# Kernel tuning notes

Measured on AMD Instinct MI355X. Metric: run time of the kernel, lower is better.

## Reference

```python
import jax, jax.numpy as jnp
import numpy as np

DIM = 128; NH = 4; HD = DIM // NH; WS = 7; SS = 3
H1, W1 = 64, 32            # int(256/(224/56)), int(128/(224/56))
PAD_B = (WS - H1 % WS) % WS
PAD_R = (WS - W1 % WS) % WS
H, W = H1 + PAD_B, W1 + PAD_R   # 70, 35
NWIN = (H // WS) * (W // WS)    # 50 windows
N = WS * WS                      # 49 tokens per window
SCALE = HD ** -0.5


def _rel_pos_index():
    c = np.stack(np.meshgrid(np.arange(WS), np.arange(WS), indexing='ij')).reshape(2, -1)
    r = (c[:, :, None] - c[:, None, :]).transpose(1, 2, 0)
    r[:, :, 0] += WS - 1; r[:, :, 1] += WS - 1; r[:, :, 0] *= 2 * WS - 1
    return jnp.asarray(r.sum(-1))  # [N, N] int


def _attn_mask():
    img = np.zeros((H, W), np.float32); cnt = 0
    for h0, h1 in [(0, H - WS), (H - WS, H - SS), (H - SS, H)]:
        for w0, w1 in [(0, W - WS), (W - WS, W - SS), (W - SS, W)]:
            img[h0:h1, w0:w1] = cnt; cnt += 1
    mw = img.reshape(H // WS, WS, W // WS, WS).transpose(0, 2, 1, 3).reshape(-1, N)
    am = mw[:, None, :] - mw[:, :, None]
    return jnp.asarray(np.where(am != 0, -100.0, 0.0).astype(np.float32))  # [NWIN, N, N]


REL_IDX = _rel_pos_index()
ATTN_MASK = _attn_mask()


def _ln(x, g, b):
    m = x.mean(-1, keepdims=True)
    v = jnp.var(x, axis=-1, keepdims=True)
    return (x - m) * jax.lax.rsqrt(v + 1e-5) * g + b


def setup_inputs() -> dict:
    key = jax.random.key(0)
    ks = jax.random.split(key, 8)
    s = 0.02
    return {
        'x': jax.random.normal(ks[0], (64, H1 * W1, DIM), jnp.float32),
        'norm1_g': jnp.ones((DIM,), jnp.float32),
        'norm1_b': jnp.zeros((DIM,), jnp.float32),
        'qkv_w': jax.random.normal(ks[1], (DIM, 3 * DIM), jnp.float32) * s,
        'qkv_b': jnp.zeros((3 * DIM,), jnp.float32),
        'rpb': jax.random.normal(ks[2], ((2 * WS - 1) ** 2, NH), jnp.float32) * s,
        'proj_w': jax.random.normal(ks[3], (DIM, DIM), jnp.float32) * s,
        'proj_b': jnp.zeros((DIM,), jnp.float32),
        'norm2_g': jnp.ones((DIM,), jnp.float32),
        'norm2_b': jnp.zeros((DIM,), jnp.float32),
        'fc1_w': jax.random.normal(ks[4], (DIM, 4 * DIM), jnp.float32) * s,
        'fc1_b': jnp.zeros((4 * DIM,), jnp.float32),
        'fc2_w': jax.random.normal(ks[5], (4 * DIM, DIM), jnp.float32) * s,
        'fc2_b': jnp.zeros((DIM,), jnp.float32),
    }


def reference(x, norm1_g, norm1_b, qkv_w, qkv_b, rpb, proj_w, proj_b,
              norm2_g, norm2_b, fc1_w, fc1_b, fc2_w, fc2_b):
    B, L, C = x.shape
    x = x.reshape(B, H1, W1, C)
    x = jnp.pad(x, ((0, 0), (0, PAD_B), (0, PAD_R), (0, 0)))  # [B,H,W,C]
    shortcut = x.reshape(B, H * W, C)
    xn = _ln(shortcut, norm1_g, norm1_b).reshape(B, H, W, C)
    # cyclic shift
    xs = jnp.roll(xn, (-SS, -SS), axis=(1, 2))
    # window partition -> [B*NWIN, N, C]
    xw = xs.reshape(B, H // WS, WS, W // WS, WS, C).transpose(0, 1, 3, 2, 4, 5).reshape(B * NWIN, N, C)
    # windowed multi-head attention
    qkv = (xw @ qkv_w + qkv_b).reshape(B * NWIN, N, 3, NH, HD).transpose(2, 0, 3, 1, 4)
    q, k, v = qkv[0] * SCALE, qkv[1], qkv[2]            # [B*NWIN, NH, N, HD]
    attn = jnp.einsum('whnd,whmd->whnm', q, k)
    bias = rpb[REL_IDX].transpose(2, 0, 1)              # [NH, N, N]
    attn = attn + bias[None]
    attn = attn.reshape(B, NWIN, NH, N, N) + ATTN_MASK[None, :, None]
    attn = jax.nn.softmax(attn, axis=-1).reshape(B * NWIN, NH, N, N)
    out = jnp.einsum('whnm,whmd->whnd', attn, v).transpose(0, 2, 1, 3).reshape(B * NWIN, N, C)
    out = out @ proj_w + proj_b
    # window reverse + reverse shift
    out = out.reshape(B, H // WS, W // WS, WS, WS, C).transpose(0, 1, 3, 2, 4, 5).reshape(B, H, W, C)
    out = jnp.roll(out, (SS, SS), axis=(1, 2)).reshape(B, H * W, C)
    x = shortcut + out
    # MLP (exact GELU, matching torch default)
    h = _ln(x, norm2_g, norm2_b)
    h = jax.nn.gelu(h @ fc1_w + fc1_b, approximate=False) @ fc2_w + fc2_b
    x = x + h
    # remove padding
    return x.reshape(B, H, W, C)[:, :H1, :W1, :].reshape(B, H1 * W1, C)
```

## Files before the change

kernel.cpp:

```cpp
#include <hip/hip_runtime.h>
#include <hip/hip_bf16.h>

#define B_ 64
#define H1_ 64
#define W1_ 32
#define Hp 70
#define Wp 35
#define C_ 128
#define NH_ 4
#define HD_ 32
#define WS_ 7
#define SS_ 3
#define NWC_ 5
#define NWIN_ 50
#define NTOK_ 49
#define SCALE_ 0.17677669529663687f

typedef __hip_bfloat16 bf16;
typedef __attribute__((ext_vector_type(8))) short sh8;
typedef __attribute__((ext_vector_type(4))) float f32x4;

__device__ __forceinline__ float bs2f(short s) {
    unsigned int u = ((unsigned int)(unsigned short)s) << 16;
    float f; __builtin_memcpy(&f, &u, 4); return f;
}
__device__ __forceinline__ short f2bs(float f) {
    bf16 h = __float2bfloat16(f);
    return *reinterpret_cast<short*>(&h);
}

__global__ void prep_k(const float* __restrict__ qkvw, const float* __restrict__ projw,
                       const float* __restrict__ f1w, const float* __restrict__ f2w,
                       const float* __restrict__ rpb,
                       short* __restrict__ ws) {
    int tid = blockIdx.x * 256 + threadIdx.x;
    if (tid < 49152) {
        int n = tid >> 7, k = tid & 127;
        ws[tid] = f2bs(qkvw[k*384 + n]);
    } else if (tid < 65536) {
        int t = tid - 49152; int n = t >> 7, k = t & 127;
        ws[tid] = f2bs(projw[k*128 + n]);
    } else if (tid < 131072) {
        int t = tid - 65536; int n = t >> 7, k = t & 127;
        ws[tid] = f2bs(f1w[k*512 + n]);
    } else if (tid < 196608) {
        int t = tid - 131072; int n = t >> 9, k = t & 511;
        ws[tid] = f2bs(f2w[k*128 + n]);
    } else if (tid < 212992) {
        int t = tid - 196608;
        int h = t >> 12, i = (t >> 6) & 63, j = t & 63;
        float val = -30000.f;
        if (i < NTOK_ && j < NTOK_) {
            int ri = i / WS_, ci = i % WS_, rj = j / WS_, cj = j % WS_;
            val = rpb[((ri - rj + 6)*13 + (ci - cj + 6))*4 + h];
        }
        ws[tid] = f2bs(val);
    }
}

__global__ __launch_bounds__(512, 4) void win_attn(
    const float* __restrict__ x,
    const float* __restrict__ n1g, const float* __restrict__ n1b,
    const float* __restrict__ qkvb, const short* __restrict__ bt,
    const float* __restrict__ projb,
    const short* __restrict__ wq, const short* __restrict__ wp,
    float* __restrict__ out)
{
    __shared__ char smem[71680];
    short* q_s = (short*)smem;
    short* k_s = (short*)(smem + 17408);
    short* cat = (short*)(smem + 17408);
    short* vt  = (short*)(smem + 34816);
    short* xsp = (short*)(smem + 53248);
    short* p_s = (short*)(smem + 53248);

    const int tid = threadIdx.x;
    const int lane = tid & 63, wv = tid >> 6;
    const int l15 = lane & 15, l4 = lane >> 4;
    const int mt = wv & 3, hg = wv >> 2;
    const int bw = blockIdx.x;
    const int b = bw / NWIN_, win = bw % NWIN_;
    const int wr = win / NWC_, wc = win % NWC_;

    #pragma unroll
    for (int it = 0; it < 4; ++it) {
        int n = it*16 + wv*2 + (lane >> 5);
        int r = n / WS_, cc = n % WS_;
        int h = (wr*WS_ + r + SS_) % Hp;
        int w = (wc*WS_ + cc + SS_) % Wp;
        int c0 = (lane & 31) * 4;
        float4 v = make_float4(0.f, 0.f, 0.f, 0.f);
        if (n < NTOK_ && h < H1_ && w < W1_)
            v = *(const float4*)(x + ((size_t)(b*H1_*W1_ + h*W1_ + w))*C_ + c0);
        float s  = v.x + v.y + v.z + v.w;
        float sq = v.x*v.x + v.y*v.y + v.z*v.z + v.w*v.w;
        #pragma unroll
        for (int off = 1; off < 32; off <<= 1) {
            s  += __shfl_xor(s, off);
            sq += __shfl_xor(sq, off);
        }
        float mean = s * (1.f/128.f);
        float var  = sq * (1.f/128.f) - mean*mean;
        float rstd = rsqrtf(var + 1e-5f);
        short4 o;
        o.x = f2bs((v.x - mean)*rstd*n1g[c0+0] + n1b[c0+0]);
        o.y = f2bs((v.y - mean)*rstd*n1g[c0+1] + n1b[c0+1]);
        o.z = f2bs((v.z - mean)*rstd*n1g[c0+2] + n1b[c0+2]);
        o.w = f2bs((v.w - mean)*rstd*n1g[c0+3] + n1b[c0+3]);
        *(short4*)(xsp + n*136 + c0) = o;
    }
    __syncthreads();

    {
        sh8 bq[4], bqn[4];
        {
            int n0 = (wv*3)*16 + l15;
            #pragma unroll
            for (int kk = 0; kk < 4; ++kk)
                bq[kk] = *(const sh8*)(wq + n0*C_ + kk*32 + l4*8);
        }
        for (int t = 0; t < 3; ++t) {
            int n0 = (wv*3 + t)*16 + l15;
            if (t < 2) {
                int n1 = n0 + 16;
                #pragma unroll
                for (int kk = 0; kk < 4; ++kk)
                    bqn[kk] = *(const sh8*)(wq + n1*C_ + kk*32 + l4*8);
            }
            int mat = n0 >> 7, c = n0 & 127;
            float bias = qkvb[n0];
            float scl = (mat == 0) ? SCALE_ : 1.f;
            #pragma unroll
            for (int mt4 = 0; mt4 < 4; ++mt4) {
                f32x4 acc = {0.f,0.f,0.f,0.f};
                #pragma unroll
                for (int kk = 0; kk < 4; ++kk) {
                    sh8 av = *(const sh8*)(xsp + (mt4*16 + l15)*136 + kk*32 + l4*8);
                    acc = __builtin_amdgcn_mfma_f32_16x16x32_bf16(av, bq[kk], acc, 0,0,0);
                }
                #pragma unroll
                for (int r = 0; r < 4; ++r) {
                    int m0 = mt4*16 + l4*4 + r;
                    float vc = (acc[r] + bias) * scl;
                    if (mat == 0)      q_s[m0*136 + c] = f2bs(vc);
                    else if (mat == 1) k_s[m0*136 + c] = f2bs(vc);
                    else               vt[c*72 + m0]   = f2bs(vc);
                }
            }
            #pragma unroll
            for (int kk = 0; kk < 4; ++kk) bq[kk] = bqn[kk];
        }
    }
    __syncthreads();

    int zi_r[4];
    #pragma unroll
    for (int r = 0; r < 4; ++r) {
        int i = mt*16 + l4*4 + r;
        int ri = i / WS_, ci = i % WS_;
        int hi = wr*WS_ + ri, wi = wc*WS_ + ci;
        zi_r[r] = (hi < 63 ? 0 : (hi < 67 ? 1 : 2))*3 + (wi < 28 ? 0 : (wi < 32 ? 1 : 2));
    }
    int zj_n[4];
    #pragma unroll
    for (int nt = 0; nt < 4; ++nt) {
        int j = nt*16 + l15;
        int rj = j / WS_, cj = j % WS_;
        int hj = wr*WS_ + rj, wj = wc*WS_ + cj;
        zj_n[nt] = (hj < 63 ? 0 : (hj < 67 ? 1 : 2))*3 + (wj < 28 ? 0 : (wj < 32 ? 1 : 2));
    }

    short* myp = p_s + wv*16*72;
    f32x4 o_acc[2][2] = {};
    #pragma unroll
    for (int hl = 0; hl < 2; ++hl) {
        const int h = hg*2 + hl;
        sh8 aq = *(const sh8*)(q_s + (mt*16 + l15)*136 + h*HD_ + l4*8);
        f32x4 s[4];
        __builtin_amdgcn_s_setprio(1);
        #pragma unroll
        for (int nt = 0; nt < 4; ++nt) {
            sh8 bk = *(const sh8*)(k_s + (nt*16 + l15)*136 + h*HD_ + l4*8);
            f32x4 z = {0.f,0.f,0.f,0.f};
            s[nt] = __builtin_amdgcn_mfma_f32_16x16x32_bf16(aq, bk, z, 0,0,0);
        }
        __builtin_amdgcn_s_setprio(0);
        #pragma unroll
        for (int r = 0; r < 4; ++r) {
            const short* btrow = bt + ((size_t)(h*64 + mt*16 + l4*4 + r))*64 + l15;
            #pragma unroll
            for (int nt = 0; nt < 4; ++nt) {
                float sv = s[nt][r] + bs2f(btrow[nt*16]);
                if (zi_r[r] != zj_n[nt]) sv -= 100.f;
                s[nt][r] = sv;
            }
        }
        #pragma unroll
        for (int r = 0; r < 4; ++r) {
            float m0 = fmaxf(fmaxf(s[0][r], s[1][r]), fmaxf(s[2][r], s[3][r]));
            #pragma unroll
            for (int off = 1; off < 16; off <<= 1) m0 = fmaxf(m0, __shfl_xor(m0, off));
            float ls = 0.f;
            #pragma unroll
            for (int nt = 0; nt < 4; ++nt) {
                float e = __expf(s[nt][r] - m0);
                s[nt][r] = e; ls += e;
            }
            #pragma unroll
            for (int off = 1; off < 16; off <<= 1) ls += __shfl_xor(ls, off);
            float inv = 1.f / ls;
            #pragma unroll
            for (int nt = 0; nt < 4; ++nt)
                myp[(l4*4 + r)*72 + nt*16 + l15] = f2bs(s[nt][r] * inv);
        }
        sh8 ap0 = *(const sh8*)(myp + l15*72 + l4*8);
        sh8 ap1 = *(const sh8*)(myp + l15*72 + 32 + l4*8);
        __builtin_amdgcn_s_setprio(1);
        #pragma unroll
        for (int nt2 = 0; nt2 < 2; ++nt2) {
            sh8 bv0 = *(const sh8*)(vt + (h*HD_ + nt2*16 + l15)*72 + l4*8);
            sh8 bv1 = *(const sh8*)(vt + (h*HD_ + nt2*16 + l15)*72 + 32 + l4*8);
            o_acc[hl][nt2] = __builtin_amdgcn_mfma_f32_16x16x32_bf16(ap0, bv0, o_acc[hl][nt2], 0,0,0);
            o_acc[hl][nt2] = __builtin_amdgcn_mfma_f32_16x16x32_bf16(ap1, bv1, o_acc[hl][nt2], 0,0,0);
        }
        __builtin_amdgcn_s_setprio(0);
    }

    __syncthreads();

    #pragma unroll
    for (int hl = 0; hl < 2; ++hl)
        #pragma unroll
        for (int nt2 = 0; nt2 < 2; ++nt2)
            #pragma unroll
            for (int r = 0; r < 4; ++r)
                cat[(mt*16 + l4*4 + r)*136 + (hg*2+hl)*HD_ + nt2*16 + l15] = f2bs(o_acc[hl][nt2][r]);

    bool pred[4]; size_t tokb[4];
    #pragma unroll
    for (int r = 0; r < 4; ++r) {
        int m = mt*16 + l4*4 + r;
        int rr = m / WS_, cc = m % WS_;
        int hh = (wr*WS_ + rr + SS_) % Hp;
        int ww = (wc*WS_ + cc + SS_) % Wp;
        pred[r] = (m < NTOK_) && (hh < H1_) && (ww < W1_);
        tokb[r] = ((size_t)(b*H1_*W1_ + hh*W1_ + ww))*C_;
    }

    sh8 pa[4];
    #pragma unroll
    for (int kk = 0; kk < 4; ++kk)
        pa[kk] = *(const sh8*)(cat + (mt*16 + l15)*136 + kk*32 + l4*8);

    sh8 bpw[4], bpwn[4];
    #pragma unroll
    for (int kk = 0; kk < 4; ++kk)
        bpw[kk] = *(const sh8*)(wp + (hg*64 + l15)*C_ + kk*32 + l4*8);
    for (int nt = 0; nt < 4; ++nt) {
        int ch = hg*64 + nt*16 + l15;
        if (nt < 3) {
            #pragma unroll
            for (int kk = 0; kk < 4; ++kk)
                bpwn[kk] = *(const sh8*)(wp + (ch+16)*C_ + kk*32 + l4*8);
        }
        f32x4 acc = {0.f,0.f,0.f,0.f};
        #pragma unroll
        for (int kk = 0; kk < 4; ++kk)
            acc = __builtin_amdgcn_mfma_f32_16x16x32_bf16(pa[kk], bpw[kk], acc, 0,0,0);
        float pbv = projb[ch];
        #pragma unroll
        for (int r = 0; r < 4; ++r)
            if (pred[r])
                out[tokb[r] + ch] = x[tokb[r] + ch] + acc[r] + pbv;
        #pragma unroll
        for (int kk = 0; kk < 4; ++kk) bpw[kk] = bpwn[kk];
    }
}

__global__ __launch_bounds__(512) void mlp_k(
    float* __restrict__ xio,
    const float* __restrict__ n2g, const float* __restrict__ n2b,
    const float* __restrict__ f1b, const float* __restrict__ f2b,
    const short* __restrict__ w1, const short* __restrict__ w2)
{
    __shared__ char smem[51200];
    float* xin = (float*)smem;
    short* hv  = (short*)smem;
    float* outs= (float*)smem;
    short* h2  = (short*)(smem + 33792);

    const int tid = threadIdx.x;
    const int lane = tid & 63, wv = tid >> 6;
    const int l15 = lane & 15, l4 = lane >> 4;
    const int mh = wv & 1, ng = wv >> 1;
    const size_t base = (size_t)blockIdx.x * 64 * C_;

    for (int i = tid; i < 2048; i += 512) {
        float4 v = ((const float4*)(xio + base))[i];
        int row = i >> 5, col = (i & 31) * 4;
        *(float4*)(xin + row*132 + col) = v;
    }
    __syncthreads();

    {
        int tok = tid >> 3, sub = tid & 7;
        float vbuf[16];
        float s = 0.f, sq = 0.f;
        #pragma unroll
        for (int c = 0; c < 16; ++c) {
            float v = xin[tok*132 + sub*16 + c];
            vbuf[c] = v; s += v; sq += v*v;
        }
        #pragma unroll
        for (int off = 1; off < 8; off <<= 1) {
            s  += __shfl_xor(s, off);
            sq += __shfl_xor(sq, off);
        }
        float mean = s * (1.f/128.f);
        float var  = sq * (1.f/128.f) - mean*mean;
        float rstd = rsqrtf(var + 1e-5f);
        #pragma unroll
        for (int c = 0; c < 16; ++c) {
            int ch = sub*16 + c;
            h2[tok*136 + ch] = f2bs((vbuf[c] - mean)*rstd*n2g[ch] + n2b[ch]);
        }
    }
    float res[2][2][4];
    #pragma unroll
    for (int mt2 = 0; mt2 < 2; ++mt2)
        #pragma unroll
        for (int nt = 0; nt < 2; ++nt)
            #pragma unroll
            for (int r = 0; r < 4; ++r) {
                int m  = (mh*2 + mt2)*16 + l4*4 + r;
                int ch = ng*32 + nt*16 + l15;
                res[mt2][nt][r] = xin[m*132 + ch];
            }
    __syncthreads();

    f32x4 facc[2][2] = {};
    #pragma unroll 1
    for (int chunk = 0; chunk < 2; ++chunk) {
        const int c0 = chunk*256;
        {
            sh8 b1[4], b1n[4];
            #pragma unroll
            for (int kk = 0; kk < 4; ++kk)
                b1[kk] = *(const sh8*)(w1 + (size_t)(c0 + ng*64 + l15)*C_ + kk*32 + l4*8);
            for (int t = 0; t < 4; ++t) {
                int n = c0 + ng*64 + t*16 + l15;
                if (t < 3) {
                    #pragma unroll
                    for (int kk = 0; kk < 4; ++kk)
                        b1n[kk] = *(const sh8*)(w1 + (size_t)(n + 16)*C_ + kk*32 + l4*8);
                }
                float bias = f1b[n];
                #pragma unroll
                for (int mt2 = 0; mt2 < 2; ++mt2) {
                    int mrow = (mh*2 + mt2)*16;
                    f32x4 acc = {0.f,0.f,0.f,0.f};
                    #pragma unroll
                    for (int kk = 0; kk < 4; ++kk) {
                        sh8 av = *(const sh8*)(h2 + (mrow + l15)*136 + kk*32 + l4*8);
                        acc = __builtin_amdgcn_mfma_f32_16x16x32_bf16(av, b1[kk], acc, 0,0,0);
                    }
                    #pragma unroll
                    for (int r = 0; r < 4; ++r) {
                        float xv = acc[r] + bias;
                        float g = xv * 0.5f * (1.f + erff(xv * 0.70710678118654752f));
                        hv[(mrow + l4*4 + r)*264 + ng*64 + t*16 + l15] = f2bs(g);
                    }
                }
                #pragma unroll
                for (int kk = 0; kk < 4; ++kk) b1[kk] = b1n[kk];
            }
        }
        __syncthreads();
        {
            sh8 b2[2], b2n[2];
            #pragma unroll
            for (int nt = 0; nt < 2; ++nt)
                b2[nt] = *(const sh8*)(w2 + (size_t)(ng*32 + nt*16 + l15)*512 + c0 + l4*8);
            for (int ks = 0; ks < 8; ++ks) {
                if (ks < 7) {
                    #pragma unroll
                    for (int nt = 0; nt < 2; ++nt)
                        b2n[nt] = *(const sh8*)(w2 + (size_t)(ng*32 + nt*16 + l15)*512 + c0 + (ks+1)*32 + l4*8);
                }
                #pragma unroll
                for (int mt2 = 0; mt2 < 2; ++mt2) {
                    sh8 av = *(const sh8*)(hv + ((mh*2 + mt2)*16 + l15)*264 + ks*32 + l4*8);
                    facc[mt2][0] = __builtin_amdgcn_mfma_f32_16x16x32_bf16(av, b2[0], facc[mt2][0], 0,0,0);
                    facc[mt2][1] = __builtin_amdgcn_mfma_f32_16x16x32_bf16(av, b2[1], facc[mt2][1], 0,0,0);
                }
                b2[0] = b2n[0]; b2[1] = b2n[1];
            }
        }
        __syncthreads();
    }

    #pragma unroll
    for (int mt2 = 0; mt2 < 2; ++mt2)
        #pragma unroll
        for (int nt = 0; nt < 2; ++nt) {
            int oc = ng*32 + nt*16 + l15;
            float bias = f2b[oc];
            #pragma unroll
            for (int r = 0; r < 4; ++r) {
                int m = (mh*2 + mt2)*16 + l4*4 + r;
                outs[m*132 + oc] = res[mt2][nt][r] + facc[mt2][nt][r] + bias;
            }
        }
    __syncthreads();
    for (int i = tid; i < 2048; i += 512) {
        int row = i >> 5, col = (i & 31) * 4;
        ((float4*)(xio + base))[i] = *(const float4*)(outs + row*132 + col);
    }
}

extern "C" void kernel_launch(void* const* d_in, const int* in_sizes, int n_in,
                              void* d_out, int out_size, void* d_ws, size_t ws_size,
                              hipStream_t stream) {
    const float* x    = (const float*)d_in[0];
    const float* n1g  = (const float*)d_in[1];
    const float* n1b  = (const float*)d_in[2];
    const float* qkvw = (const float*)d_in[3];
    const float* qkvb = (const float*)d_in[4];
    const float* rpb  = (const float*)d_in[5];
    const float* pw   = (const float*)d_in[6];
    const float* pb   = (const float*)d_in[7];
    const float* n2g  = (const float*)d_in[8];
    const float* n2b  = (const float*)d_in[9];
    const float* f1w  = (const float*)d_in[10];
    const float* f1b  = (const float*)d_in[11];
    const float* f2w  = (const float*)d_in[12];
    const float* f2b  = (const float*)d_in[13];

    short* ws = (short*)d_ws;
    const short* wq = ws;
    const short* wp = ws + 49152;
    const short* w1 = ws + 65536;
    const short* w2 = ws + 131072;
    const short* bt = ws + 196608;
    float* xio = (float*)d_out;

    hipLaunchKernelGGL(prep_k, dim3(832), dim3(256), 0, stream, qkvw, pw, f1w, f2w, rpb, ws);
    hipLaunchKernelGGL(win_attn, dim3(B_*NWIN_), dim3(512), 0, stream,
                       x, n1g, n1b, qkvb, bt, pb, wq, wp, xio);
    hipLaunchKernelGGL(mlp_k, dim3(B_*H1_*W1_/64), dim3(512), 0, stream,
                       xio, n2g, n2b, f1b, f2b, w1, w2);
}
```

Before: 307.5 us.

## Compute transposed attention scores and pass probabilities via lane shuffles instead of LDS

Computes S^T with K as the MFMA A operand, so each lane holds a query column. Softmax then reduces over registers plus two cross-row shuffles, and the bf16 probabilities are repacked into the PV A-operand with __shfl rather than a round trip through shared memory. The bias table is stored transposed to match. The residual add of x moves from the attention epilogue into the MLP kernel's load, and an extra barrier is added after the concat write. The aim is to cut LDS traffic and shuffle-reduction steps in exchange for more cross-lane shuffles.

```diff
diff --git a/kernel.cpp b/kernel.cpp
--- a/kernel.cpp
+++ b/kernel.cpp
@@ -27,6 +27,9 @@
 __device__ __forceinline__ short f2bs(float f) {
     bf16 h = __float2bfloat16(f);
     return *reinterpret_cast<short*>(&h);
+}
+__device__ __forceinline__ unsigned pk2(float lo, float hi) {
+    return ((unsigned)(unsigned short)f2bs(hi) << 16) | (unsigned)(unsigned short)f2bs(lo);
 }
 
 __global__ void prep_k(const float* __restrict__ qkvw, const float* __restrict__ projw,
@@ -48,10 +51,10 @@
         ws[tid] = f2bs(f2w[k*128 + n]);
     } else if (tid < 212992) {
         int t = tid - 196608;
-        int h = t >> 12, i = (t >> 6) & 63, j = t & 63;
+        int h = t >> 12, k = (t >> 6) & 63, q = t & 63;
         float val = -30000.f;
-        if (i < NTOK_ && j < NTOK_) {
-            int ri = i / WS_, ci = i % WS_, rj = j / WS_, cj = j % WS_;
+        if (q < NTOK_ && k < NTOK_) {
+            int ri = q / WS_, ci = q % WS_, rj = k / WS_, cj = k % WS_;
             val = rpb[((ri - rj + 6)*13 + (ci - cj + 6))*4 + h];
         }
         ws[tid] = f2bs(val);
@@ -61,18 +64,17 @@
 __global__ __launch_bounds__(512, 4) void win_attn(
     const float* __restrict__ x,
     const float* __restrict__ n1g, const float* __restrict__ n1b,
-    const float* __restrict__ qkvb, const short* __restrict__ bt,
+    const float* __restrict__ qkvb, const short* __restrict__ btT,
     const float* __restrict__ projb,
     const short* __restrict__ wq, const short* __restrict__ wp,
     float* __restrict__ out)
 {
-    __shared__ char smem[71680];
+    __shared__ char smem[70656];
     short* q_s = (short*)smem;
     short* k_s = (short*)(smem + 17408);
     short* cat = (short*)(smem + 17408);
     short* vt  = (short*)(smem + 34816);
     short* xsp = (short*)(smem + 53248);
-    short* p_s = (short*)(smem + 53248);
 
     const int tid = threadIdx.x;
     const int lane = tid & 63, wv = tid >> 6;
@@ -153,77 +155,98 @@
     }
     __syncthreads();
 
-    int zi_r[4];
-    #pragma unroll
-    for (int r = 0; r < 4; ++r) {
-        int i = mt*16 + l4*4 + r;
-        int ri = i / WS_, ci = i % WS_;
-        int hi = wr*WS_ + ri, wi = wc*WS_ + ci;
-        zi_r[r] = (hi < 63 ? 0 : (hi < 67 ? 1 : 2))*3 + (wi < 28 ? 0 : (wi < 32 ? 1 : 2));
-    }
-    int zj_n[4];
-    #pragma unroll
-    for (int nt = 0; nt < 4; ++nt) {
-        int j = nt*16 + l15;
-        int rj = j / WS_, cj = j % WS_;
-        int hj = wr*WS_ + rj, wj = wc*WS_ + cj;
-        zj_n[nt] = (hj < 63 ? 0 : (hj < 67 ? 1 : 2))*3 + (wj < 28 ? 0 : (wj < 32 ? 1 : 2));
-    }
-
-    short* myp = p_s + wv*16*72;
+    int zq;
+    {
+        int qt = mt*16 + l15;
+        int rt = qt / WS_, ct = qt % WS_;
+        int hi = wr*WS_ + rt, wi2 = wc*WS_ + ct;
+        zq = (hi < 63 ? 0 : (hi < 67 ? 1 : 2))*3 + (wi2 < 28 ? 0 : (wi2 < 32 ? 1 : 2));
+    }
+    int zk[4][4];
+    #pragma unroll
+    for (int nt = 0; nt < 4; ++nt)
+        #pragma unroll
+        for (int r = 0; r < 4; ++r) {
+            int kt = nt*16 + l4*4 + r;
+            int rt = kt / WS_, ct = kt % WS_;
+            int hj = wr*WS_ + rt, wj = wc*WS_ + ct;
+            zk[nt][r] = (hj < 63 ? 0 : (hj < 67 ? 1 : 2))*3 + (wj < 28 ? 0 : (wj < 32 ? 1 : 2));
+        }
+
+    const int sl0 = ((l4 & 1) * 2)*16 + l15;
+    const int sl1 = sl0 + 16;
+    const bool hi4 = (l4 >> 1) != 0;
+
     f32x4 o_acc[2][2] = {};
     #pragma unroll
     for (int hl = 0; hl < 2; ++hl) {
         const int h = hg*2 + hl;
-        sh8 aq = *(const sh8*)(q_s + (mt*16 + l15)*136 + h*HD_ + l4*8);
+        sh8 qf = *(const sh8*)(q_s + (mt*16 + l15)*136 + h*HD_ + l4*8);
         f32x4 s[4];
         __builtin_amdgcn_s_setprio(1);
         #pragma unroll
         for (int nt = 0; nt < 4; ++nt) {
-            sh8 bk = *(const sh8*)(k_s + (nt*16 + l15)*136 + h*HD_ + l4*8);
+            sh8 kf = *(const sh8*)(k_s + (nt*16 + l15)*136 + h*HD_ + l4*8);
             f32x4 z = {0.f,0.f,0.f,0.f};
-            s[nt] = __builtin_amdgcn_mfma_f32_16x16x32_bf16(aq, bk, z, 0,0,0);
+            s[nt] = __builtin_amdgcn_mfma_f32_16x16x32_bf16(kf, qf, z, 0,0,0);
         }
         __builtin_amdgcn_s_setprio(0);
         #pragma unroll
-        for (int r = 0; r < 4; ++r) {
-            const short* btrow = bt + ((size_t)(h*64 + mt*16 + l4*4 + r))*64 + l15;
-            #pragma unroll
-            for (int nt = 0; nt < 4; ++nt) {
-                float sv = s[nt][r] + bs2f(btrow[nt*16]);
-                if (zi_r[r] != zj_n[nt]) sv -= 100.f;
+        for (int nt = 0; nt < 4; ++nt)
+            #pragma unroll
+            for (int r = 0; r < 4; ++r) {
+                float sv = s[nt][r]
+                    + bs2f(btT[((size_t)(h*64 + nt*16 + l4*4 + r))*64 + mt*16 + l15]);
+                if (zq != zk[nt][r]) sv -= 100.f;
                 s[nt][r] = sv;
             }
-        }
-        #pragma unroll
-        for (int r = 0; r < 4; ++r) {
-            float m0 = fmaxf(fmaxf(s[0][r], s[1][r]), fmaxf(s[2][r], s[3][r]));
-            #pragma unroll
-            for (int off = 1; off < 16; off <<= 1) m0 = fmaxf(m0, __shfl_xor(m0, off));
-            float ls = 0.f;
-            #pragma unroll
-            for (int nt = 0; nt < 4; ++nt) {
+        float m0 = s[0][0];
+        #pragma unroll
+        for (int nt = 0; nt < 4; ++nt)
+            #pragma unroll
+            for (int r = 0; r < 4; ++r) m0 = fmaxf(m0, s[nt][r]);
+        m0 = fmaxf(m0, __shfl_xor(m0, 16));
+        m0 = fmaxf(m0, __shfl_xor(m0, 32));
+        float ls = 0.f;
+        #pragma unroll
+        for (int nt = 0; nt < 4; ++nt)
+            #pragma unroll
+            for (int r = 0; r < 4; ++r) {
                 float e = __expf(s[nt][r] - m0);
                 s[nt][r] = e; ls += e;
             }
-            #pragma unroll
-            for (int off = 1; off < 16; off <<= 1) ls += __shfl_xor(ls, off);
-            float inv = 1.f / ls;
-            #pragma unroll
-            for (int nt = 0; nt < 4; ++nt)
-                myp[(l4*4 + r)*72 + nt*16 + l15] = f2bs(s[nt][r] * inv);
-        }
-        sh8 ap0 = *(const sh8*)(myp + l15*72 + l4*8);
-        sh8 ap1 = *(const sh8*)(myp + l15*72 + 32 + l4*8);
-        __builtin_amdgcn_s_setprio(1);
-        #pragma unroll
-        for (int nt2 = 0; nt2 < 2; ++nt2) {
-            sh8 bv0 = *(const sh8*)(vt + (h*HD_ + nt2*16 + l15)*72 + l4*8);
-            sh8 bv1 = *(const sh8*)(vt + (h*HD_ + nt2*16 + l15)*72 + 32 + l4*8);
-            o_acc[hl][nt2] = __builtin_amdgcn_mfma_f32_16x16x32_bf16(ap0, bv0, o_acc[hl][nt2], 0,0,0);
-            o_acc[hl][nt2] = __builtin_amdgcn_mfma_f32_16x16x32_bf16(ap1, bv1, o_acc[hl][nt2], 0,0,0);
-        }
-        __builtin_amdgcn_s_setprio(0);
+        ls += __shfl_xor(ls, 16);
+        ls += __shfl_xor(ls, 32);
+        float inv = 1.f / ls;
+        unsigned p01[4], p23[4];
+        #pragma unroll
+        for (int nt = 0; nt < 4; ++nt) {
+            p01[nt] = pk2(s[nt][0]*inv, s[nt][1]*inv);
+            p23[nt] = pk2(s[nt][2]*inv, s[nt][3]*inv);
+        }
+        #pragma unroll
+        for (int ks = 0; ks < 2; ++ks) {
+            unsigned u01_lo = __shfl(p01[2*ks],   sl0);
+            unsigned u01_hi = __shfl(p01[2*ks+1], sl0);
+            unsigned u23_lo = __shfl(p23[2*ks],   sl0);
+            unsigned u23_hi = __shfl(p23[2*ks+1], sl0);
+            unsigned v01_lo = __shfl(p01[2*ks],   sl1);
+            unsigned v01_hi = __shfl(p01[2*ks+1], sl1);
+            unsigned v23_lo = __shfl(p23[2*ks],   sl1);
+            unsigned v23_hi = __shfl(p23[2*ks+1], sl1);
+            unsigned a01 = hi4 ? u01_hi : u01_lo;
+            unsigned a23 = hi4 ? u23_hi : u23_lo;
+            unsigned a45 = hi4 ? v01_hi : v01_lo;
+            unsigned a67 = hi4 ? v23_hi : v23_lo;
+            int w4[4] = {(int)a01, (int)a23, (int)a45, (int)a67};
+            sh8 ap; __builtin_memcpy(&ap, w4, 16);
+            sh8 bv0 = *(const sh8*)(vt + (h*HD_ + l15)*72      + ks*32 + l4*8);
+            sh8 bv1 = *(const sh8*)(vt + (h*HD_ + 16 + l15)*72 + ks*32 + l4*8);
+            __builtin_amdgcn_s_setprio(1);
+            o_acc[hl][0] = __builtin_amdgcn_mfma_f32_16x16x32_bf16(ap, bv0, o_acc[hl][0], 0,0,0);
+            o_acc[hl][1] = __builtin_amdgcn_mfma_f32_16x16x32_bf16(ap, bv1, o_acc[hl][1], 0,0,0);
+            __builtin_amdgcn_s_setprio(0);
+        }
     }
 
     __syncthreads();
@@ -235,6 +258,7 @@
             #pragma unroll
             for (int r = 0; r < 4; ++r)
                 cat[(mt*16 + l4*4 + r)*136 + (hg*2+hl)*HD_ + nt2*16 + l15] = f2bs(o_acc[hl][nt2][r]);
+    __syncthreads();
 
     bool pred[4]; size_t tokb[4];
     #pragma unroll
@@ -271,13 +295,14 @@
         #pragma unroll
         for (int r = 0; r < 4; ++r)
             if (pred[r])
-                out[tokb[r] + ch] = x[tokb[r] + ch] + acc[r] + pbv;
+                out[tokb[r] + ch] = acc[r] + pbv;
         #pragma unroll
         for (int kk = 0; kk < 4; ++kk) bpw[kk] = bpwn[kk];
     }
 }
 
 __global__ __launch_bounds__(512) void mlp_k(
+    const float* __restrict__ x,
     float* __restrict__ xio,
     const float* __restrict__ n2g, const float* __restrict__ n2b,
     const float* __restrict__ f1b, const float* __restrict__ f2b,
@@ -296,9 +321,11 @@
     const size_t base = (size_t)blockIdx.x * 64 * C_;
 
     for (int i = tid; i < 2048; i += 512) {
-        float4 v = ((const float4*)(xio + base))[i];
+        float4 vx = ((const float4*)(x + base))[i];
+        float4 va = ((const float4*)(xio + base))[i];
+        vx.x += va.x; vx.y += va.y; vx.z += va.z; vx.w += va.w;
         int row = i >> 5, col = (i & 31) * 4;
-        *(float4*)(xin + row*132 + col) = v;
+        *(float4*)(xin + row*132 + col) = vx;
     }
     __syncthreads();
 
@@ -448,5 +475,5 @@
     hipLaunchKernelGGL(win_attn, dim3(B_*NWIN_), dim3(512), 0, stream,
                        x, n1g, n1b, qkvb, bt, pb, wq, wp, xio);
     hipLaunchKernelGGL(mlp_k, dim3(B_*H1_*W1_/64), dim3(512), 0, stream,
-                       xio, n2g, n2b, f1b, f2b, w1, w2);
-}
+                       x, xio, n2g, n2b, f1b, f2b, w1, w2);
+}
```

After: 311.4 us. No clear change (+1.3%).
